# Performance work log

Hardware: AMD Instinct MI355X
Metric: run time of the kernel (lower is better)

Reference implementation:

```python
import jax, jax.numpy as jnp
import numpy as np

B, K, H, W = 16, 64, 128, 128


def _centroid(hm):
    # hm: [B, K, H, W] -> rounded soft-argmax keypoints [B, K, 2] (x, y)
    zeta = hm.sum(axis=(2, 3))                                   # [B, K]
    xs = jnp.arange(hm.shape[3], dtype=hm.dtype)                 # j index (width)
    ys = jnp.arange(hm.shape[2], dtype=hm.dtype)                 # i index (height)
    kp_x = jnp.einsum('bkhw,w->bk', hm, xs)                      # Sum j*v
    kp_y = jnp.einsum('bkhw,h->bk', hm, ys)                      # Sum i*v
    return jnp.stack([jnp.round(kp_x / zeta), jnp.round(kp_y / zeta)], axis=-1)


def setup_inputs() -> dict:
    key = jax.random.key(0)
    k1, k2 = jax.random.split(key)
    return {
        'combined_hm_preds': jax.random.uniform(k1, (B, K, H, W), dtype=jnp.float32),
        'tf_combined_hm_preds': jax.random.uniform(k2, (B, K, H, W), dtype=jnp.float32),
        'num_of_kp': K,
    }


def reference(combined_hm_preds, tf_combined_hm_preds, num_of_kp):
    keypoint = _centroid(combined_hm_preds)        # [B, K, 2]
    tf_keypoint = _centroid(tf_combined_hm_preds)  # [B, K, 2]
    return keypoint, tf_keypoint
```

## Files before the change

### kernel.cpp

```cpp
#include <hip/hip_runtime.h>
#include <math.h>


#define HM_H 128
#define HM_W 128

__global__ __launch_bounds__(256) void centroid_kernel(
    const float* __restrict__ hm0,
    const float* __restrict__ hm1,
    float* __restrict__ out,
    int BK)
{
    const int unit  = blockIdx.x;
    const int which = (unit >= BK) ? 1 : 0;
    const int bk    = which ? (unit - BK) : unit;

    const float* __restrict__ src =
        (which ? hm1 : hm0) + (size_t)bk * (HM_H * HM_W);
    float* __restrict__ dst = out + (size_t)which * (size_t)BK * 2 + (size_t)bk * 2;

    const int t = threadIdx.x;

    float s = 0.0f;
    float sx = 0.0f;
    float sy = 0.0f;

    const float4* __restrict__ p = (const float4*)src;
#pragma unroll
    for (int it = 0; it < 16; ++it) {
        const int f4 = t + it * 256;
        const float4 v = p[f4];
        const int fe = f4 << 2;
        const float h = (float)(fe >> 7);
        const float w = (float)(fe & 127);
        const float sv = v.x + v.y + v.z + v.w;
        s  += sv;
        sy += h * sv;
        sx += w * sv + (v.y + 2.0f * v.z + 3.0f * v.w);
    }

#pragma unroll
    for (int off = 32; off > 0; off >>= 1) {
        s  += __shfl_down(s,  off, 64);
        sx += __shfl_down(sx, off, 64);
        sy += __shfl_down(sy, off, 64);
    }

    __shared__ float ls[4], lx[4], ly[4];
    const int wid  = t >> 6;
    const int lane = t & 63;
    if (lane == 0) { ls[wid] = s; lx[wid] = sx; ly[wid] = sy; }
    __syncthreads();

    if (t == 0) {
        const float S = ls[0] + ls[1] + ls[2] + ls[3];
        const float X = lx[0] + lx[1] + lx[2] + lx[3];
        const float Y = ly[0] + ly[1] + ly[2] + ly[3];
        dst[0] = rintf(X / S);
        dst[1] = rintf(Y / S);
    }
}

extern "C" void kernel_launch(void* const* d_in, const int* in_sizes, int n_in,
                              void* d_out, int out_size, void* d_ws, size_t ws_size,
                              hipStream_t stream) {
    const float* hm0 = (const float*)d_in[0];
    const float* hm1 = (const float*)d_in[1];
    float* out = (float*)d_out;

    const int BK = out_size / 4;
    const int grid = 2 * BK;

    centroid_kernel<<<grid, 256, 0, stream>>>(hm0, hm1, out, BK);
}
```

Baseline: 146.6 us.

## Split each heatmap across four blocks with a second reduction kernel

Each heatmap reduction is now split across four blocks. Each block loads 4 float4 per thread and writes partial sums (S, X, Y) to workspace, and a second small kernel combines the partials and writes the rounded centroids. This raises the grid from 2048 to 8192 blocks and cuts the per-thread serial work. In exchange it adds a second kernel launch and a workspace round trip. The row/column index math is reworked algebraically for the new partition.

After: 144.8 us. Within noise of the previous version (-1.3%).

```diff
diff --git a/kernel.cpp b/kernel.cpp
--- a/kernel.cpp
+++ b/kernel.cpp
@@ -4,40 +4,45 @@
 
 #define HM_H 128
 #define HM_W 128
+#define PARTS 4
 
-__global__ __launch_bounds__(256) void centroid_kernel(
+__global__ __launch_bounds__(256) void centroid_partial(
     const float* __restrict__ hm0,
     const float* __restrict__ hm1,
-    float* __restrict__ out,
+    float* __restrict__ ws,
     int BK)
 {
-    const int unit  = blockIdx.x;
-    const int which = (unit >= BK) ? 1 : 0;
-    const int bk    = which ? (unit - BK) : unit;
+    const int gb   = blockIdx.x;
+    const int part = gb & (PARTS - 1);
+    const int u    = gb >> 2;
+    const int bk   = (u >= BK) ? (u - BK) : u;
+    const float* __restrict__ src =
+        ((u >= BK) ? hm1 : hm0) + (size_t)bk * (HM_H * HM_W);
 
-    const float* __restrict__ src =
-        (which ? hm1 : hm0) + (size_t)bk * (HM_H * HM_W);
-    float* __restrict__ dst = out + (size_t)which * (size_t)BK * 2 + (size_t)bk * 2;
-
+    const float4* __restrict__ p = (const float4*)src + part * 1024;
     const int t = threadIdx.x;
 
-    float s = 0.0f;
-    float sx = 0.0f;
-    float sy = 0.0f;
+    const float4 v0 = p[t];
+    const float4 v1 = p[t + 256];
+    const float4 v2 = p[t + 512];
+    const float4 v3 = p[t + 768];
 
-    const float4* __restrict__ p = (const float4*)src;
-#pragma unroll
-    for (int it = 0; it < 16; ++it) {
-        const int f4 = t + it * 256;
-        const float4 v = p[f4];
-        const int fe = f4 << 2;
-        const float h = (float)(fe >> 7);
-        const float w = (float)(fe & 127);
-        const float sv = v.x + v.y + v.z + v.w;
-        s  += sv;
-        sy += h * sv;
-        sx += w * sv + (v.y + 2.0f * v.z + 3.0f * v.w);
-    }
+    const float wbase = (float)((t << 2) & (HM_W - 1));
+    const float rl = (float)(t >> 5);
+
+    const float sv0 = v0.x + v0.y + v0.z + v0.w;
+    const float sv1 = v1.x + v1.y + v1.z + v1.w;
+    const float sv2 = v2.x + v2.y + v2.z + v2.w;
+    const float sv3 = v3.x + v3.y + v3.z + v3.w;
+
+    float s  = sv0 + sv1 + sv2 + sv3;
+    float sx = wbase * s
+             + (v0.y + v1.y + v2.y + v3.y)
+             + 2.0f * (v0.z + v1.z + v2.z + v3.z)
+             + 3.0f * (v0.w + v1.w + v2.w + v3.w);
+    float sy = rl * (sv0 + sv1 + sv2 + sv3)
+             + 8.0f * (sv1 + 2.0f * sv2 + 3.0f * sv3)
+             + (float)(part * 32) * s;
 
 #pragma unroll
     for (int off = 32; off > 0; off >>= 1) {
@@ -53,12 +58,29 @@
     __syncthreads();
 
     if (t == 0) {
-        const float S = ls[0] + ls[1] + ls[2] + ls[3];
-        const float X = lx[0] + lx[1] + lx[2] + lx[3];
-        const float Y = ly[0] + ly[1] + ly[2] + ly[3];
-        dst[0] = rintf(X / S);
-        dst[1] = rintf(Y / S);
+        ws[gb * 3 + 0] = ls[0] + ls[1] + ls[2] + ls[3];
+        ws[gb * 3 + 1] = lx[0] + lx[1] + lx[2] + lx[3];
+        ws[gb * 3 + 2] = ly[0] + ly[1] + ly[2] + ly[3];
     }
+}
+
+__global__ __launch_bounds__(256) void centroid_final(
+    const float* __restrict__ ws,
+    float* __restrict__ out,
+    int nunits)
+{
+    const int u = blockIdx.x * 256 + threadIdx.x;
+    if (u >= nunits) return;
+    const float* __restrict__ w = ws + (size_t)u * (PARTS * 3);
+    float S = 0.0f, X = 0.0f, Y = 0.0f;
+#pragma unroll
+    for (int pr = 0; pr < PARTS; ++pr) {
+        S += w[pr * 3 + 0];
+        X += w[pr * 3 + 1];
+        Y += w[pr * 3 + 2];
+    }
+    out[u * 2 + 0] = rintf(X / S);
+    out[u * 2 + 1] = rintf(Y / S);
 }
 
 extern "C" void kernel_launch(void* const* d_in, const int* in_sizes, int n_in,
@@ -67,9 +89,12 @@
     const float* hm0 = (const float*)d_in[0];
     const float* hm1 = (const float*)d_in[1];
     float* out = (float*)d_out;
+    float* ws  = (float*)d_ws;
 
-    const int BK = out_size / 4;
-    const int grid = 2 * BK;
+    const int BK     = out_size / 4;
+    const int nunits = 2 * BK;
+    const int grid1  = nunits * PARTS;
 
-    centroid_kernel<<<grid, 256, 0, stream>>>(hm0, hm1, out, BK);
+    centroid_partial<<<grid1, 256, 0, stream>>>(hm0, hm1, ws, BK);
+    centroid_final<<<(nunits + 255) / 256, 256, 0, stream>>>(ws, out, nunits);
 }
```
